# Performance work log

Measured on AMD Instinct MI355X. Metric: run time of the kernel, lower is better.

## Reference

```python
import jax, jax.numpy as jnp
import numpy as np

N_HEADS = 8
N_POINTS = 4


def _bilinear_sample(img, x, y):
    """img: (d, H, W); x, y: (P, H, W) float pixel coords (align_corners=True).
    Zero padding for out-of-bounds (matches F.grid_sample defaults).
    Returns (d, P, H, W)."""
    Hh, Ww = img.shape[1], img.shape[2]
    x0f = jnp.floor(x); y0f = jnp.floor(y)
    x0 = x0f.astype(jnp.int32); x1 = x0 + 1
    y0 = y0f.astype(jnp.int32); y1 = y0 + 1
    wx = x - x0f; wy = y - y0f

    def gather(yi, xi):
        valid = (yi >= 0) & (yi < Hh) & (xi >= 0) & (xi < Ww)
        yc = jnp.clip(yi, 0, Hh - 1)
        xc = jnp.clip(xi, 0, Ww - 1)
        v = img[:, yc, xc]  # (d, P, H, W)
        return v * valid[None].astype(img.dtype)

    out = (gather(y0, x0) * ((1 - wy) * (1 - wx))[None]
           + gather(y0, x1) * ((1 - wy) * wx)[None]
           + gather(y1, x0) * (wy * (1 - wx))[None]
           + gather(y1, x1) * (wy * wx)[None])
    return out


def _forward(query, key, W_off, b_off, W_proj, b_proj):
    B, C, H, W = query.shape
    nh, npts = N_HEADS, N_POINTS
    dh = C // nh
    N = H * W

    # offsets + weights from flattened query tokens
    qf = query.reshape(B, C, N).transpose(0, 2, 1)            # (B, N, C)
    ow = qf @ W_off + b_off                                    # (B, N, nh*npts*3)
    ow = ow.reshape(B, H, W, nh, npts, 3)
    offsets = ow[..., :2]                                      # (B,H,W,nh,npts,2)
    weights = jax.nn.softmax(ow[..., 2], axis=-1)              # (B,H,W,nh,npts)

    # base grid in [-1, 1], (x, y) order
    gy = jnp.linspace(-1.0, 1.0, H, dtype=query.dtype)
    gx = jnp.linspace(-1.0, 1.0, W, dtype=query.dtype)
    gyy, gxx = jnp.meshgrid(gy, gx, indexing='ij')             # (H, W)
    grid = jnp.stack([gxx, gyy], axis=-1)                      # (H, W, 2)

    locs = grid[None, :, :, None, None, :] + offsets * 0.1     # (B,H,W,nh,npts,2)
    locs = locs.transpose(0, 3, 4, 1, 2, 5)                    # (B,nh,npts,H,W,2)
    locs = locs.reshape(B * nh, npts, H, W, 2)

    # normalized -> pixel coords (align_corners=True)
    xpix = (locs[..., 0] + 1.0) * 0.5 * (W - 1)                # (B*nh, npts, H, W)
    ypix = (locs[..., 1] + 1.0) * 0.5 * (H - 1)

    key_r = key.reshape(B * nh, dh, H, W)
    sampled = jax.vmap(_bilinear_sample)(key_r, xpix, ypix)    # (B*nh, dh, npts, H, W)
    sampled = sampled.reshape(B, nh, dh, npts, H, W).transpose(0, 1, 3, 2, 4, 5)  # (B,nh,npts,dh,H,W)

    w = weights.transpose(0, 3, 4, 1, 2)[:, :, :, None, :, :]  # (B,nh,npts,1,H,W)
    out_feat = (sampled * w).sum(axis=2)                       # (B,nh,dh,H,W)
    out_feat = out_feat.reshape(B, C, N).transpose(0, 2, 1)    # (B,N,C)
    return out_feat @ W_proj + b_proj                          # (B,N,C)


def setup_inputs() -> dict:
    key0 = jax.random.key(0)
    ks = jax.random.split(key0, 6)
    B, C, H, W = 8, 256, 64, 64
    query = jax.random.normal(ks[0], (B, C, H, W), dtype=jnp.float32)
    key = jax.random.normal(ks[1], (B, C, H, W), dtype=jnp.float32)
    # small random offset net so sampling deviates from base grid (orig inits to 0)
    W_off = jax.random.normal(ks[2], (C, N_HEADS * N_POINTS * 3), dtype=jnp.float32) * 0.01
    b_off = jax.random.normal(ks[3], (N_HEADS * N_POINTS * 3,), dtype=jnp.float32) * 0.01
    W_proj = jax.random.normal(ks[4], (C, C), dtype=jnp.float32) * (1.0 / np.sqrt(C))
    b_proj = jnp.zeros((C,), dtype=jnp.float32)
    return {"query": query, "key": key, "W_off": W_off, "b_off": b_off,
            "W_proj": W_proj, "b_proj": b_proj}


def reference(query, key, W_off, b_off, W_proj, b_proj):
    return _forward(query, key, W_off, b_off, W_proj, b_proj)
```

## Files before the change

kernel.cpp:

```cpp
#include <hip/hip_runtime.h>

#define NH   8
#define NPTS 4
#define BB   8
#define CCH  256
#define HH   64
#define WW   64
#define NPIX 4096
#define DH   32

__global__ __launch_bounds__(256)
void kA_offsets(const float* __restrict__ query, const float* __restrict__ W_off,
                const float* __restrict__ b_off, float4* __restrict__ coords)
{
    __shared__ float q_lds[64][64];
    __shared__ float w_lds[64][96];

    const int t  = threadIdx.x;
    const int g0 = blockIdx.x * 64;
    const int b  = g0 >> 12;
    const int n0 = g0 & (NPIX - 1);
    const float* qbase = query + (size_t)b * CCH * NPIX;

    const int px = t & 63;
    const int jg = t >> 6;
    const int j0 = jg * 24;

    float acc[24];
#pragma unroll
    for (int i = 0; i < 24; ++i) acc[i] = 0.f;

    for (int kc = 0; kc < CCH; kc += 64) {
        const int p4 = (t & 15) << 2;
        const int k0 = t >> 4;
#pragma unroll
        for (int kk = 0; kk < 64; kk += 16) {
            float4 v = *(const float4*)(qbase + (size_t)(kc + k0 + kk) * NPIX + (n0 + p4));
            *(float4*)&q_lds[k0 + kk][p4] = v;
        }
#pragma unroll
        for (int ii = 0; ii < 6; ++ii) {
            int i4 = t + ii * 256;
            int k  = i4 / 24;
            int j4 = i4 - k * 24;
            *(float4*)&w_lds[k][j4 << 2] =
                *(const float4*)(W_off + (size_t)(kc + k) * 96 + (j4 << 2));
        }
        __syncthreads();
#pragma unroll 8
        for (int k = 0; k < 64; ++k) {
            float a = q_lds[k][px];
#pragma unroll
            for (int j4 = 0; j4 < 6; ++j4) {
                float4 w = *(const float4*)&w_lds[k][j0 + (j4 << 2)];
                acc[j4 * 4 + 0] = fmaf(a, w.x, acc[j4 * 4 + 0]);
                acc[j4 * 4 + 1] = fmaf(a, w.y, acc[j4 * 4 + 1]);
                acc[j4 * 4 + 2] = fmaf(a, w.z, acc[j4 * 4 + 2]);
                acc[j4 * 4 + 3] = fmaf(a, w.w, acc[j4 * 4 + 3]);
            }
        }
        __syncthreads();
    }

    const int n = n0 + px;
    const int x = n & 63;
    const int y = n >> 6;
    const float fx = (float)x, fy = (float)y;

#pragma unroll
    for (int hh = 0; hh < 2; ++hh) {
        const int head = jg * 2 + hh;
        const int lb   = hh * 12;
        float ox[4], oy[4], l[4];
#pragma unroll
        for (int p = 0; p < 4; ++p) {
            ox[p] = acc[lb + p * 3 + 0] + b_off[j0 + lb + p * 3 + 0];
            oy[p] = acc[lb + p * 3 + 1] + b_off[j0 + lb + p * 3 + 1];
            l[p]  = acc[lb + p * 3 + 2] + b_off[j0 + lb + p * 3 + 2];
        }
        float m = fmaxf(fmaxf(l[0], l[1]), fmaxf(l[2], l[3]));
        float e[4], s = 0.f;
#pragma unroll
        for (int p = 0; p < 4; ++p) { e[p] = __expf(l[p] - m); s += e[p]; }
        float inv = 1.f / s;
        float4* cp = coords + ((size_t)(b * NPIX + n) * NH + head) * NPTS;
#pragma unroll
        for (int p = 0; p < 4; ++p) {
            cp[p] = make_float4(fx + ox[p] * 3.15f, fy + oy[p] * 3.15f, e[p] * inv, 0.f);
        }
    }
}

__global__ __launch_bounds__(256)
void kT_transpose(const float* __restrict__ key, float* __restrict__ keyT)
{
    __shared__ float tile[64][65];
    int bid = blockIdx.x;
    const int nt = bid & 63; bid >>= 6;
    const int ct = bid & 3;  bid >>= 2;
    const int b  = bid;
    const int n0 = nt * 64, c0 = ct * 64;
    const int t = threadIdx.x;

    const float* src = key + ((size_t)b * CCH + c0) * NPIX + n0;
#pragma unroll
    for (int ii = 0; ii < 4; ++ii) {
        int idx = t + ii * 256;
        int cc = idx >> 4, q = idx & 15;
        float4 v = *(const float4*)(src + (size_t)cc * NPIX + (q << 2));
        tile[cc][(q << 2) + 0] = v.x;
        tile[cc][(q << 2) + 1] = v.y;
        tile[cc][(q << 2) + 2] = v.z;
        tile[cc][(q << 2) + 3] = v.w;
    }
    __syncthreads();
    float* dst = keyT + ((size_t)(b * NPIX + n0)) * CCH + c0;
#pragma unroll
    for (int ii = 0; ii < 4; ++ii) {
        int idx = t + ii * 256;
        int nn = idx >> 4, q = idx & 15;
        float4 v = make_float4(tile[(q << 2) + 0][nn], tile[(q << 2) + 1][nn],
                               tile[(q << 2) + 2][nn], tile[(q << 2) + 3][nn]);
        *(float4*)(dst + (size_t)nn * CCH + (q << 2)) = v;
    }
}

__global__ __launch_bounds__(256)
void kB_gather(const float* __restrict__ keyT, const float4* __restrict__ coords,
               float* __restrict__ feat)
{
    const int bid  = blockIdx.x;
    const int sbid = (bid & 7) * 1024 + (bid >> 3);

    const int t  = threadIdx.x;
    const int wv = t >> 6, l = t & 63;
    const int g  = sbid * 4 + wv;
    const int b  = g >> 12;
    const int head = l >> 3;
    const int cl   = (l & 7) << 2;
    const int c    = head * DH + cl;

    const float*  kb = keyT + (((size_t)b << 12)) * CCH;
    const float4* cp = coords + ((size_t)g * NH + head) * NPTS;

    float4 acc = make_float4(0.f, 0.f, 0.f, 0.f);
#pragma unroll
    for (int pt = 0; pt < 4; ++pt) {
        float4 co = cp[pt];
        float xp = co.x, yp = co.y, wgt = co.z;
        float x0f = floorf(xp), y0f = floorf(yp);
        int   x0  = (int)x0f,  y0  = (int)y0f;
        float wx  = xp - x0f,  wy  = yp - y0f;
#pragma unroll
        for (int cr = 0; cr < 4; ++cr) {
            int   xi = x0 + (cr & 1);
            int   yi = y0 + (cr >> 1);
            float wc = ((cr & 1) ? wx : 1.f - wx) * ((cr >> 1) ? wy : 1.f - wy);
            bool  valid = (xi >= 0) && (xi < WW) && (yi >= 0) && (yi < HH);
            int   xc = min(max(xi, 0), WW - 1);
            int   yc = min(max(yi, 0), HH - 1);
            float ww = valid ? (wgt * wc) : 0.f;
            float4 v = *(const float4*)(kb + ((size_t)((yc << 6) + xc)) * CCH + c);
            acc.x = fmaf(ww, v.x, acc.x);
            acc.y = fmaf(ww, v.y, acc.y);
            acc.z = fmaf(ww, v.z, acc.z);
            acc.w = fmaf(ww, v.w, acc.w);
        }
    }
    *(float4*)(feat + (size_t)g * CCH + c) = acc;
}

__global__ __launch_bounds__(256)
void kB_sample(const float* __restrict__ key, const float4* __restrict__ coords,
               float* __restrict__ feat)
{
    __shared__ float cx[4][64], cy[4][64], cw[4][64];

    const int t = threadIdx.x;
    int bi = blockIdx.x;
    const int y    = bi & 63; bi >>= 6;
    const int head = bi & 7;  bi >>= 3;
    const int b    = bi;

    {
        const int xx = t >> 2, pt = t & 3;
        float4 v = coords[((size_t)(b * NPIX + y * WW + xx) * NH + head) * NPTS + pt];
        cx[pt][xx] = v.x; cy[pt][xx] = v.y; cw[pt][xx] = v.z;
    }
    __syncthreads();

    const int x  = t & 63;
    const int cg = t >> 6;
    const int c0 = head * DH + cg * 8;
    const float* kbase = key + ((size_t)b * CCH + c0) * NPIX;

    float acc[8];
#pragma unroll
    for (int i = 0; i < 8; ++i) acc[i] = 0.f;

#pragma unroll
    for (int pt = 0; pt < 4; ++pt) {
        float xp = cx[pt][x], yp = cy[pt][x], wgt = cw[pt][x];
        float x0f = floorf(xp), y0f = floorf(yp);
        int   x0  = (int)x0f,  y0  = (int)y0f;
        float wx  = xp - x0f,  wy  = yp - y0f;
#pragma unroll
        for (int cr = 0; cr < 4; ++cr) {
            int   xi = x0 + (cr & 1);
            int   yi = y0 + (cr >> 1);
            float wc = ((cr & 1) ? wx : 1.f - wx) * ((cr >> 1) ? wy : 1.f - wy);
            bool  valid = (xi >= 0) && (xi < WW) && (yi >= 0) && (yi < HH);
            int   xc = min(max(xi, 0), WW - 1);
            int   yc = min(max(yi, 0), HH - 1);
            const float* p = kbase + yc * WW + xc;
            float ww = valid ? (wgt * wc) : 0.f;
#pragma unroll
            for (int c = 0; c < 8; ++c)
                acc[c] = fmaf(ww, p[(size_t)c * NPIX], acc[c]);
        }
    }

    float* fp = feat + (size_t)(b * NPIX + y * WW + x) * CCH + c0;
    *(float4*)fp       = make_float4(acc[0], acc[1], acc[2], acc[3]);
    *(float4*)(fp + 4) = make_float4(acc[4], acc[5], acc[6], acc[7]);
}

__global__ __launch_bounds__(256)
void kC_proj(const float* __restrict__ feat, const float* __restrict__ W_proj,
             const float* __restrict__ b_proj, float* __restrict__ out)
{
    __shared__ float a_lds[32][64];
    __shared__ float b_lds[32][128];

    const int t  = threadIdx.x;
    const int mb = blockIdx.x >> 1;
    const int nb = blockIdx.x & 1;
    const int m0 = mb * 64, n0 = nb * 128;

    const int tm = t >> 4, tn = t & 15;

    float acc[4][8];
#pragma unroll
    for (int i = 0; i < 4; ++i)
#pragma unroll
        for (int j = 0; j < 8; ++j) acc[i][j] = 0.f;

    for (int kc = 0; kc < 256; kc += 32) {
        float4 a[2];
#pragma unroll
        for (int ii = 0; ii < 2; ++ii) {
            int idx = t + ii * 256;
            int r = idx >> 3, q = idx & 7;
            a[ii] = *(const float4*)(feat + (size_t)(m0 + r) * 256 + kc + (q << 2));
        }
        float4 w[4];
#pragma unroll
        for (int ii = 0; ii < 4; ++ii) {
            int idx = t + ii * 256;
            int kk = idx >> 5, q = idx & 31;
            w[ii] = *(const float4*)(W_proj + (size_t)(kc + kk) * 256 + n0 + (q << 2));
        }
        __syncthreads();
#pragma unroll
        for (int ii = 0; ii < 2; ++ii) {
            int idx = t + ii * 256;
            int r = idx >> 3, q = idx & 7;
            a_lds[(q << 2) + 0][r] = a[ii].x;
            a_lds[(q << 2) + 1][r] = a[ii].y;
            a_lds[(q << 2) + 2][r] = a[ii].z;
            a_lds[(q << 2) + 3][r] = a[ii].w;
        }
#pragma unroll
        for (int ii = 0; ii < 4; ++ii) {
            int idx = t + ii * 256;
            int kk = idx >> 5, q = idx & 31;
            *(float4*)&b_lds[kk][q << 2] = w[ii];
        }
        __syncthreads();
#pragma unroll
        for (int k = 0; k < 32; ++k) {
            float4 av  = *(const float4*)&a_lds[k][tm << 2];
            float4 bv0 = *(const float4*)&b_lds[k][tn << 2];
            float4 bv1 = *(const float4*)&b_lds[k][64 + (tn << 2)];
            acc[0][0] = fmaf(av.x, bv0.x, acc[0][0]);
            acc[0][1] = fmaf(av.x, bv0.y, acc[0][1]);
            acc[0][2] = fmaf(av.x, bv0.z, acc[0][2]);
            acc[0][3] = fmaf(av.x, bv0.w, acc[0][3]);
            acc[0][4] = fmaf(av.x, bv1.x, acc[0][4]);
            acc[0][5] = fmaf(av.x, bv1.y, acc[0][5]);
            acc[0][6] = fmaf(av.x, bv1.z, acc[0][6]);
            acc[0][7] = fmaf(av.x, bv1.w, acc[0][7]);
            acc[1][0] = fmaf(av.y, bv0.x, acc[1][0]);
            acc[1][1] = fmaf(av.y, bv0.y, acc[1][1]);
            acc[1][2] = fmaf(av.y, bv0.z, acc[1][2]);
            acc[1][3] = fmaf(av.y, bv0.w, acc[1][3]);
            acc[1][4] = fmaf(av.y, bv1.x, acc[1][4]);
            acc[1][5] = fmaf(av.y, bv1.y, acc[1][5]);
            acc[1][6] = fmaf(av.y, bv1.z, acc[1][6]);
            acc[1][7] = fmaf(av.y, bv1.w, acc[1][7]);
            acc[2][0] = fmaf(av.z, bv0.x, acc[2][0]);
            acc[2][1] = fmaf(av.z, bv0.y, acc[2][1]);
            acc[2][2] = fmaf(av.z, bv0.z, acc[2][2]);
            acc[2][3] = fmaf(av.z, bv0.w, acc[2][3]);
            acc[2][4] = fmaf(av.z, bv1.x, acc[2][4]);
            acc[2][5] = fmaf(av.z, bv1.y, acc[2][5]);
            acc[2][6] = fmaf(av.z, bv1.z, acc[2][6]);
            acc[2][7] = fmaf(av.z, bv1.w, acc[2][7]);
            acc[3][0] = fmaf(av.w, bv0.x, acc[3][0]);
            acc[3][1] = fmaf(av.w, bv0.y, acc[3][1]);
            acc[3][2] = fmaf(av.w, bv0.z, acc[3][2]);
            acc[3][3] = fmaf(av.w, bv0.w, acc[3][3]);
            acc[3][4] = fmaf(av.w, bv1.x, acc[3][4]);
            acc[3][5] = fmaf(av.w, bv1.y, acc[3][5]);
            acc[3][6] = fmaf(av.w, bv1.z, acc[3][6]);
            acc[3][7] = fmaf(av.w, bv1.w, acc[3][7]);
        }
        __syncthreads();
    }

    const float4 bp0 = *(const float4*)(b_proj + n0 + (tn << 2));
    const float4 bp1 = *(const float4*)(b_proj + n0 + 64 + (tn << 2));
#pragma unroll
    for (int i = 0; i < 4; ++i) {
        float* op = out + (size_t)(m0 + (tm << 2) + i) * 256 + n0;
        *(float4*)(op + (tn << 2)) =
            make_float4(acc[i][0] + bp0.x, acc[i][1] + bp0.y,
                        acc[i][2] + bp0.z, acc[i][3] + bp0.w);
        *(float4*)(op + 64 + (tn << 2)) =
            make_float4(acc[i][4] + bp1.x, acc[i][5] + bp1.y,
                        acc[i][6] + bp1.z, acc[i][7] + bp1.w);
    }
}

extern "C" void kernel_launch(void* const* d_in, const int* in_sizes, int n_in,
                              void* d_out, int out_size, void* d_ws, size_t ws_size,
                              hipStream_t stream)
{
    const float* query  = (const float*)d_in[0];
    const float* key    = (const float*)d_in[1];
    const float* W_off  = (const float*)d_in[2];
    const float* b_off  = (const float*)d_in[3];
    const float* W_proj = (const float*)d_in[4];
    const float* b_proj = (const float*)d_in[5];
    float* out = (float*)d_out;

    const size_t keyT_bytes   = (size_t)BB * NPIX * CCH * sizeof(float);
    const size_t coords_bytes = (size_t)BB * NPIX * NH * NPTS * sizeof(float4);
    const size_t feat_bytes   = (size_t)BB * NPIX * CCH * sizeof(float);

    if (ws_size >= keyT_bytes + coords_bytes + feat_bytes) {
        float*  keyT   = (float*)d_ws;
        float4* coords = (float4*)((char*)d_ws + keyT_bytes);
        float*  feat   = (float*)((char*)d_ws + keyT_bytes + coords_bytes);

        kA_offsets<<<(BB * NPIX) / 64, 256, 0, stream>>>(query, W_off, b_off, coords);
        kT_transpose<<<BB * 4 * 64, 256, 0, stream>>>(key, keyT);
        kB_gather<<<(BB * NPIX) / 4, 256, 0, stream>>>(keyT, coords, feat);
        kC_proj<<<(BB * NPIX / 64) * 2, 256, 0, stream>>>(feat, W_proj, b_proj, out);
    } else {
        float4* coords = (float4*)d_ws;
        float*  feat   = (float*)((char*)d_ws + coords_bytes);

        kA_offsets<<<(BB * NPIX) / 64, 256, 0, stream>>>(query, W_off, b_off, coords);
        kB_sample<<<BB * NH * HH, 256, 0, stream>>>(key, coords, feat);
        kC_proj<<<(BB * NPIX / 64) * 2, 256, 0, stream>>>(feat, W_proj, b_proj, out);
    }
}
```

Baseline: 253.0 us.

## Enlarge projection GEMM tile to 128x128 and read query directly in offsets kernel

The projection GEMM now computes a 128x128 output tile per block with an 8x8 register tile per thread, halving the block count and increasing reuse of each LDS load. The A tile is padded to reduce bank conflicts, and the trailing barrier is dropped because loads are staged through registers before the next sync. The offsets kernel stops staging query in LDS and reads the column straight from global memory, which removes a barrier-bound copy but relies on coalesced per-k loads. The larger accumulator raises register pressure and may lower occupancy.

```diff
diff --git a/kernel.cpp b/kernel.cpp
--- a/kernel.cpp
+++ b/kernel.cpp
@@ -13,31 +13,24 @@
 void kA_offsets(const float* __restrict__ query, const float* __restrict__ W_off,
                 const float* __restrict__ b_off, float4* __restrict__ coords)
 {
-    __shared__ float q_lds[64][64];
     __shared__ float w_lds[64][96];
 
     const int t  = threadIdx.x;
     const int g0 = blockIdx.x * 64;
     const int b  = g0 >> 12;
     const int n0 = g0 & (NPIX - 1);
-    const float* qbase = query + (size_t)b * CCH * NPIX;
 
     const int px = t & 63;
     const int jg = t >> 6;
     const int j0 = jg * 24;
 
+    const float* qcol = query + (size_t)b * CCH * NPIX + n0 + px;
+
     float acc[24];
 #pragma unroll
     for (int i = 0; i < 24; ++i) acc[i] = 0.f;
 
     for (int kc = 0; kc < CCH; kc += 64) {
-        const int p4 = (t & 15) << 2;
-        const int k0 = t >> 4;
-#pragma unroll
-        for (int kk = 0; kk < 64; kk += 16) {
-            float4 v = *(const float4*)(qbase + (size_t)(kc + k0 + kk) * NPIX + (n0 + p4));
-            *(float4*)&q_lds[k0 + kk][p4] = v;
-        }
 #pragma unroll
         for (int ii = 0; ii < 6; ++ii) {
             int i4 = t + ii * 256;
@@ -49,7 +42,7 @@
         __syncthreads();
 #pragma unroll 8
         for (int k = 0; k < 64; ++k) {
-            float a = q_lds[k][px];
+            float a = qcol[(size_t)(kc + k) * NPIX];
 #pragma unroll
             for (int j4 = 0; j4 < 6; ++j4) {
                 float4 w = *(const float4*)&w_lds[k][j0 + (j4 << 2)];
@@ -229,106 +222,75 @@
 void kC_proj(const float* __restrict__ feat, const float* __restrict__ W_proj,
              const float* __restrict__ b_proj, float* __restrict__ out)
 {
-    __shared__ float a_lds[32][64];
+    __shared__ float a_lds[32][132];
     __shared__ float b_lds[32][128];
 
     const int t  = threadIdx.x;
     const int mb = blockIdx.x >> 1;
     const int nb = blockIdx.x & 1;
-    const int m0 = mb * 64, n0 = nb * 128;
+    const int m0 = mb * 128, n0 = nb * 128;
 
     const int tm = t >> 4, tn = t & 15;
-
-    float acc[4][8];
-#pragma unroll
-    for (int i = 0; i < 4; ++i)
+    const int ra = t >> 3, qa = t & 7;
+    const int kb = t >> 5, qb = t & 31;
+
+    float acc[8][8];
+#pragma unroll
+    for (int i = 0; i < 8; ++i)
 #pragma unroll
         for (int j = 0; j < 8; ++j) acc[i][j] = 0.f;
 
     for (int kc = 0; kc < 256; kc += 32) {
-        float4 a[2];
-#pragma unroll
-        for (int ii = 0; ii < 2; ++ii) {
-            int idx = t + ii * 256;
-            int r = idx >> 3, q = idx & 7;
-            a[ii] = *(const float4*)(feat + (size_t)(m0 + r) * 256 + kc + (q << 2));
-        }
+        float4 a[4];
+#pragma unroll
+        for (int ii = 0; ii < 4; ++ii)
+            a[ii] = *(const float4*)(feat + (size_t)(m0 + ra + ii * 32) * 256 + kc + (qa << 2));
         float4 w[4];
 #pragma unroll
+        for (int ii = 0; ii < 4; ++ii)
+            w[ii] = *(const float4*)(W_proj + (size_t)(kc + kb + ii * 8) * 256 + n0 + (qb << 2));
+        __syncthreads();
+#pragma unroll
         for (int ii = 0; ii < 4; ++ii) {
-            int idx = t + ii * 256;
-            int kk = idx >> 5, q = idx & 31;
-            w[ii] = *(const float4*)(W_proj + (size_t)(kc + kk) * 256 + n0 + (q << 2));
-        }
+            const int r = ra + ii * 32;
+            a_lds[(qa << 2) + 0][r] = a[ii].x;
+            a_lds[(qa << 2) + 1][r] = a[ii].y;
+            a_lds[(qa << 2) + 2][r] = a[ii].z;
+            a_lds[(qa << 2) + 3][r] = a[ii].w;
+        }
+#pragma unroll
+        for (int ii = 0; ii < 4; ++ii)
+            *(float4*)&b_lds[kb + ii * 8][qb << 2] = w[ii];
         __syncthreads();
 #pragma unroll
-        for (int ii = 0; ii < 2; ++ii) {
-            int idx = t + ii * 256;
-            int r = idx >> 3, q = idx & 7;
-            a_lds[(q << 2) + 0][r] = a[ii].x;
-            a_lds[(q << 2) + 1][r] = a[ii].y;
-            a_lds[(q << 2) + 2][r] = a[ii].z;
-            a_lds[(q << 2) + 3][r] = a[ii].w;
-        }
-#pragma unroll
-        for (int ii = 0; ii < 4; ++ii) {
-            int idx = t + ii * 256;
-            int kk = idx >> 5, q = idx & 31;
-            *(float4*)&b_lds[kk][q << 2] = w[ii];
-        }
-        __syncthreads();
-#pragma unroll
         for (int k = 0; k < 32; ++k) {
-            float4 av  = *(const float4*)&a_lds[k][tm << 2];
+            float4 av0 = *(const float4*)&a_lds[k][tm << 2];
+            float4 av1 = *(const float4*)&a_lds[k][64 + (tm << 2)];
             float4 bv0 = *(const float4*)&b_lds[k][tn << 2];
             float4 bv1 = *(const float4*)&b_lds[k][64 + (tn << 2)];
-            acc[0][0] = fmaf(av.x, bv0.x, acc[0][0]);
-            acc[0][1] = fmaf(av.x, bv0.y, acc[0][1]);
-            acc[0][2] = fmaf(av.x, bv0.z, acc[0][2]);
-            acc[0][3] = fmaf(av.x, bv0.w, acc[0][3]);
-            acc[0][4] = fmaf(av.x, bv1.x, acc[0][4]);
-            acc[0][5] = fmaf(av.x, bv1.y, acc[0][5]);
-            acc[0][6] = fmaf(av.x, bv1.z, acc[0][6]);
-            acc[0][7] = fmaf(av.x, bv1.w, acc[0][7]);
-            acc[1][0] = fmaf(av.y, bv0.x, acc[1][0]);
-            acc[1][1] = fmaf(av.y, bv0.y, acc[1][1]);
-            acc[1][2] = fmaf(av.y, bv0.z, acc[1][2]);
-            acc[1][3] = fmaf(av.y, bv0.w, acc[1][3]);
-            acc[1][4] = fmaf(av.y, bv1.x, acc[1][4]);
-            acc[1][5] = fmaf(av.y, bv1.y, acc[1][5]);
-            acc[1][6] = fmaf(av.y, bv1.z, acc[1][6]);
-            acc[1][7] = fmaf(av.y, bv1.w, acc[1][7]);
-            acc[2][0] = fmaf(av.z, bv0.x, acc[2][0]);
-            acc[2][1] = fmaf(av.z, bv0.y, acc[2][1]);
-            acc[2][2] = fmaf(av.z, bv0.z, acc[2][2]);
-            acc[2][3] = fmaf(av.z, bv0.w, acc[2][3]);
-            acc[2][4] = fmaf(av.z, bv1.x, acc[2][4]);
-            acc[2][5] = fmaf(av.z, bv1.y, acc[2][5]);
-            acc[2][6] = fmaf(av.z, bv1.z, acc[2][6]);
-            acc[2][7] = fmaf(av.z, bv1.w, acc[2][7]);
-            acc[3][0] = fmaf(av.w, bv0.x, acc[3][0]);
-            acc[3][1] = fmaf(av.w, bv0.y, acc[3][1]);
-            acc[3][2] = fmaf(av.w, bv0.z, acc[3][2]);
-            acc[3][3] = fmaf(av.w, bv0.w, acc[3][3]);
-            acc[3][4] = fmaf(av.w, bv1.x, acc[3][4]);
-            acc[3][5] = fmaf(av.w, bv1.y, acc[3][5]);
-            acc[3][6] = fmaf(av.w, bv1.z, acc[3][6]);
-            acc[3][7] = fmaf(av.w, bv1.w, acc[3][7]);
-        }
-        __syncthreads();
+            float ar[8] = {av0.x, av0.y, av0.z, av0.w, av1.x, av1.y, av1.z, av1.w};
+            float br[8] = {bv0.x, bv0.y, bv0.z, bv0.w, bv1.x, bv1.y, bv1.z, bv1.w};
+#pragma unroll
+            for (int i = 0; i < 8; ++i)
+#pragma unroll
+                for (int j = 0; j < 8; ++j)
+                    acc[i][j] = fmaf(ar[i], br[j], acc[i][j]);
+        }
     }
 
     const float4 bp0 = *(const float4*)(b_proj + n0 + (tn << 2));
     const float4 bp1 = *(const float4*)(b_proj + n0 + 64 + (tn << 2));
-#pragma unroll
-    for (int i = 0; i < 4; ++i) {
-        float* op = out + (size_t)(m0 + (tm << 2) + i) * 256 + n0;
+    const float bpr[8] = {bp0.x, bp0.y, bp0.z, bp0.w, bp1.x, bp1.y, bp1.z, bp1.w};
+#pragma unroll
+    for (int i = 0; i < 8; ++i) {
+        const int m = m0 + ((i < 4) ? 0 : 64) + (tm << 2) + (i & 3);
+        float* op = out + (size_t)m * 256 + n0;
         *(float4*)(op + (tn << 2)) =
-            make_float4(acc[i][0] + bp0.x, acc[i][1] + bp0.y,
-                        acc[i][2] + bp0.z, acc[i][3] + bp0.w);
+            make_float4(acc[i][0] + bpr[0], acc[i][1] + bpr[1],
+                        acc[i][2] + bpr[2], acc[i][3] + bpr[3]);
         *(float4*)(op + 64 + (tn << 2)) =
-            make_float4(acc[i][4] + bp1.x, acc[i][5] + bp1.y,
-                        acc[i][6] + bp1.z, acc[i][7] + bp1.w);
+            make_float4(acc[i][4] + bpr[4], acc[i][5] + bpr[5],
+                        acc[i][6] + bpr[6], acc[i][7] + bpr[7]);
     }
 }
 
@@ -356,13 +318,13 @@
         kA_offsets<<<(BB * NPIX) / 64, 256, 0, stream>>>(query, W_off, b_off, coords);
         kT_transpose<<<BB * 4 * 64, 256, 0, stream>>>(key, keyT);
         kB_gather<<<(BB * NPIX) / 4, 256, 0, stream>>>(keyT, coords, feat);
-        kC_proj<<<(BB * NPIX / 64) * 2, 256, 0, stream>>>(feat, W_proj, b_proj, out);
+        kC_proj<<<(BB * NPIX / 128) * 2, 256, 0, stream>>>(feat, W_proj, b_proj, out);
     } else {
         float4* coords = (float4*)d_ws;
         float*  feat   = (float*)((char*)d_ws + coords_bytes);
 
         kA_offsets<<<(BB * NPIX) / 64, 256, 0, stream>>>(query, W_off, b_off, coords);
         kB_sample<<<BB * NH * HH, 256, 0, stream>>>(key, coords, feat);
-        kC_proj<<<(BB * NPIX / 64) * 2, 256, 0, stream>>>(feat, W_proj, b_proj, out);
-    }
-}
+        kC_proj<<<(BB * NPIX / 128) * 2, 256, 0, stream>>>(feat, W_proj, b_proj, out);
+    }
+}
```

Result: slower. 277.7 us (+9.8%).
